# Kernel tuning notes

Hardware: AMD Instinct MI355X
Metric: run time of the kernel (lower is better)

## Reference

```python
import jax, jax.numpy as jnp
import numpy as np

B, S, D = 64, 512, 768
NEG = -1e30


def setup_inputs() -> dict:
    key = jax.random.key(0)
    ks = jax.random.split(key, 20)
    def rn(k, shape, scale=0.02):
        return jax.random.normal(k, shape, dtype=jnp.float32) * scale
    ep = jax.random.randint(ks[1], (B, 3, 2), 0, S, dtype=jnp.int32)
    return {
        "encoding": jax.random.normal(ks[0], (B, S, D), dtype=jnp.float32),
        "ent_pos": jnp.sort(ep, axis=-1),
        "Ar_W": rn(ks[2], (5, D)), "Ar_b": rn(ks[3], (D,)),
        "Vr_W1": rn(ks[4], (2 * D, 512)), "Vr_b1": rn(ks[5], (512,)),
        "Vr_W2": rn(ks[6], (512, 5)), "Vr_b2": rn(ks[7], (5,)),
        "gate_W": rn(ks[8], (2 * D, D)), "gate_b": rn(ks[9], (D,)),
        "pred_W1": rn(ks[10], (3 * D, 512)), "pred_b1": rn(ks[11], (512,)),
        "pred_W2": rn(ks[12], (512, 5)), "pred_b2": rn(ks[13], (5,)),
        "proj_W": rn(ks[14], (D, 1)), "proj_b": rn(ks[15], (1,)),
    }


def reference(encoding, ent_pos, Ar_W, Ar_b, Vr_W1, Vr_b1, Vr_W2, Vr_b2,
              gate_W, gate_b, pred_W1, pred_b1, pred_W2, pred_b2, proj_W, proj_b):
    # --- entity span max-pooling (vectorized over batch & 3 entities) ---
    pos = jnp.arange(S)                                   # [S]
    start = ent_pos[..., 0:1]                             # [B,3,1]
    end = ent_pos[..., 1:2]                               # [B,3,1]
    mask = (pos >= start) & (pos <= end)                  # [B,3,S]
    ent = jnp.max(jnp.where(mask[..., None], encoding[:, None, :, :], NEG), axis=2)  # [B,3,D]
    # dropout layers are identity at inference

    def vr(a, b):  # V_r_layer: Linear(1536,512)+ReLU+Linear(512,5)+Sigmoid
        h = jax.nn.relu(jnp.concatenate([a, b], axis=-1) @ Vr_W1 + Vr_b1)
        return jax.nn.sigmoid(h @ Vr_W2 + Vr_b2)          # [B,5]

    def gate(u, e):  # gated residual update
        g = jax.nn.sigmoid(jnp.concatenate([u, e], axis=-1) @ gate_W + gate_b)
        return g * e + (1.0 - g) * u

    e1, e2, e3 = ent[:, 0], ent[:, 1], ent[:, 2]          # [B,D] each
    for _ in range(5):
        u1 = (vr(e2, e3) @ Ar_W + Ar_b) * e1
        u2 = (vr(e1, e3) @ Ar_W + Ar_b) * e2
        u3 = (vr(e1, e2) @ Ar_W + Ar_b) * e3
        e1, e2, e3 = gate(u1, e1), gate(u2, e2), gate(u3, e3)
    final_ent = jnp.stack([e1, e2, e3], axis=1)           # [B,3,D]

    # predict_layer on the ORIGINAL pooled entity embeddings (per source code)
    flat = ent.reshape(B, 3 * D)
    rel = jax.nn.relu(flat @ pred_W1 + pred_b1) @ pred_W2 + pred_b2  # [B,5]
    ent_score = jax.nn.sigmoid(ent @ proj_W + proj_b)[..., 0]       # [B,3]
    return rel, ent_score, final_ent
```

## Files before the change

kernel.cpp:

```cpp
#include <hip/hip_runtime.h>
#include <hip/hip_bf16.h>
#include <math.h>

#define NEGF (-1e30f)

#define ENT_OFF  1179648u
#define EA_OFF   1327104u
#define EB_OFF   1474560u
#define SP_OFF   1622016u
#define PP_OFF   1637376u

__device__ __forceinline__ float sigmoidf_(float x){ return 1.0f/(1.0f+expf(-x)); }

__global__ __launch_bounds__(192) void k_span(
    const float* __restrict__ enc, const int* __restrict__ ent_pos,
    const float* __restrict__ projW, const float* __restrict__ projb,
    float* __restrict__ ws, float* __restrict__ out)
{
    __shared__ float red[4];
    int bi = blockIdx.x; int t = threadIdx.x;
    int b = bi/3;
    int st = ent_pos[bi*2+0], en = ent_pos[bi*2+1];
    float4 m = make_float4(NEGF,NEGF,NEGF,NEGF);
    const float4* e4 = (const float4*)enc + (size_t)b*512*192 + t;
    int r = st;
    for (; r+3<=en; r+=4){
        float4 v0 = e4[(size_t)(r  )*192];
        float4 v1 = e4[(size_t)(r+1)*192];
        float4 v2 = e4[(size_t)(r+2)*192];
        float4 v3 = e4[(size_t)(r+3)*192];
        m.x=fmaxf(m.x,fmaxf(fmaxf(v0.x,v1.x),fmaxf(v2.x,v3.x)));
        m.y=fmaxf(m.y,fmaxf(fmaxf(v0.y,v1.y),fmaxf(v2.y,v3.y)));
        m.z=fmaxf(m.z,fmaxf(fmaxf(v0.z,v1.z),fmaxf(v2.z,v3.z)));
        m.w=fmaxf(m.w,fmaxf(fmaxf(v0.w,v1.w),fmaxf(v2.w,v3.w)));
    }
    for (; r<=en; ++r){
        float4 v = e4[(size_t)r*192];
        m.x=fmaxf(m.x,v.x); m.y=fmaxf(m.y,v.y); m.z=fmaxf(m.z,v.z); m.w=fmaxf(m.w,v.w);
    }
    ((float4*)(ws+ENT_OFF))[bi*192+t] = m;
    ((float4*)(ws+EA_OFF))[bi*192+t] = m;
    float4 w = ((const float4*)projW)[t];
    float v = m.x*w.x + m.y*w.y + m.z*w.z + m.w*w.w;
    v += __shfl_down(v, 32);
    v += __shfl_down(v, 16);
    v += __shfl_down(v, 8);
    v += __shfl_down(v, 4);
    v += __shfl_down(v, 2);
    v += __shfl_down(v, 1);
    if ((t & 63) == 0) red[t>>6] = v;
    __syncthreads();
    if (t==0) out[320 + bi] = sigmoidf_(red[0]+red[1]+red[2] + projb[0]);
}

__global__ __launch_bounds__(256) void k_pred_part(
    const float* __restrict__ predW1, float* __restrict__ ws)
{
    int ct = blockIdx.x, rb = blockIdx.y, ks = blockIdx.z;
    int tx = threadIdx.x & 31, ty = threadIdx.x >> 5;
    int row = rb*8+ty, col = ct*32+tx;
    const float* A = ws + ENT_OFF + (size_t)row*2304 + ks*288;
    const float* W = predW1 + (size_t)(ks*288)*512 + col;
    float acc = 0.f;
    #pragma unroll 4
    for (int k=0;k<288;++k){ acc = fmaf(A[k], W[(size_t)k*512], acc); }
    ws[PP_OFF + ((size_t)(ks*64+row))*512 + col] = acc;
}

__global__ __launch_bounds__(256) void k_vr_fused(
    const float* __restrict__ W1, const float* __restrict__ b1,
    const float* __restrict__ W2, const float* __restrict__ eSrc,
    const float* __restrict__ pb1, const float* __restrict__ pW2,
    const float* __restrict__ pb2,
    float* __restrict__ ws, float* __restrict__ out)
{
    __shared__ float eL[4608];
    __shared__ float red[16*16*17];
    int g = blockIdx.x;
    int t = threadIdx.x;
    if (g >= 256){
        int bx = g - 256;
        int gid = t >> 5, l = t & 31;
        int b = bx*8 + gid;
        float acc0=0,acc1=0,acc2=0,acc3=0,acc4=0;
        for (int c = l; c < 512; c += 32){
            float h = 0.f;
            #pragma unroll
            for (int ks=0;ks<8;++ks) h += ws[PP_OFF + ((size_t)(ks*64+b))*512 + c];
            h = fmaxf(h + pb1[c], 0.f);
            acc0 = fmaf(h, pW2[c*5+0], acc0);
            acc1 = fmaf(h, pW2[c*5+1], acc1);
            acc2 = fmaf(h, pW2[c*5+2], acc2);
            acc3 = fmaf(h, pW2[c*5+3], acc3);
            acc4 = fmaf(h, pW2[c*5+4], acc4);
        }
        #pragma unroll
        for (int s=16; s>0; s>>=1){
            acc0 += __shfl_down(acc0, s, 32);
            acc1 += __shfl_down(acc1, s, 32);
            acc2 += __shfl_down(acc2, s, 32);
            acc3 += __shfl_down(acc3, s, 32);
            acc4 += __shfl_down(acc4, s, 32);
        }
        if (l == 0){
            out[b*5+0] = acc0 + pb2[0];
            out[b*5+1] = acc1 + pb2[1];
            out[b*5+2] = acc2 + pb2[2];
            out[b*5+3] = acc3 + pb2[3];
            out[b*5+4] = acc4 + pb2[4];
        }
        return;
    }
    int ct = g & 7, bg = g >> 3;
    int b0 = bg*2;
    const float* eBase = eSrc + (size_t)b0*2304;
    for (int idx=t; idx<4608; idx+=256) eL[idx] = eBase[idx];
    __syncthreads();

    int tp = t & 15;
    int kq = t >> 4;
    int c0 = ct*64;
    int col = c0 + 4*tp;
    const float* Wp = W1 + (size_t)(kq*96)*512 + col;
    int off1 = (kq<8) ? (768 + kq*96) : (1536 + (kq-8)*96);
    int off2 = (kq<8) ? (      kq*96) : (768  + (kq-8)*96);
    const float* pP0 = eL + off1;
    const float* pQ0 = eL + off2;
    const float* pP1 = eL + 2304 + off1;
    const float* pQ1 = eL + 2304 + off2;
    float aP0[4]={0,0,0,0}, aQ0[4]={0,0,0,0}, aP1[4]={0,0,0,0}, aQ1[4]={0,0,0,0};
    #pragma unroll 8
    for (int i=0;i<96;++i){
        float4 w = *(const float4*)(Wp + (size_t)i*512);
        float p0 = pP0[i], q0 = pQ0[i], p1 = pP1[i], q1 = pQ1[i];
        aP0[0]=fmaf(p0,w.x,aP0[0]); aP0[1]=fmaf(p0,w.y,aP0[1]); aP0[2]=fmaf(p0,w.z,aP0[2]); aP0[3]=fmaf(p0,w.w,aP0[3]);
        aQ0[0]=fmaf(q0,w.x,aQ0[0]); aQ0[1]=fmaf(q0,w.y,aQ0[1]); aQ0[2]=fmaf(q0,w.z,aQ0[2]); aQ0[3]=fmaf(q0,w.w,aQ0[3]);
        aP1[0]=fmaf(p1,w.x,aP1[0]); aP1[1]=fmaf(p1,w.y,aP1[1]); aP1[2]=fmaf(p1,w.z,aP1[2]); aP1[3]=fmaf(p1,w.w,aP1[3]);
        aQ1[0]=fmaf(q1,w.x,aQ1[0]); aQ1[1]=fmaf(q1,w.y,aQ1[1]); aQ1[2]=fmaf(q1,w.z,aQ1[2]); aQ1[3]=fmaf(q1,w.w,aQ1[3]);
    }
    float* rp = red + (kq*16 + tp)*17;
    #pragma unroll
    for (int c=0;c<4;++c){ rp[c]=aP0[c]; rp[4+c]=aQ0[c]; rp[8+c]=aP1[c]; rp[12+c]=aQ1[c]; }
    __syncthreads();

    if (t < 128){
        int bb = t >> 6;
        int tc = t & 63;
        int tp2 = tc >> 2, c = tc & 3;
        int base = bb*8;
        float SP1=0,SP2=0,SQ1=0,SQ2=0;
        #pragma unroll
        for (int k=0;k<8;++k){
            SP1 += red[(k*16+tp2)*17 + base + c];
            SQ1 += red[(k*16+tp2)*17 + base + 4 + c];
            SP2 += red[((k+8)*16+tp2)*17 + base + c];
            SQ2 += red[((k+8)*16+tp2)*17 + base + 4 + c];
        }
        int cc = c0 + tc;
        float bv = b1[cc];
        float h0 = fmaxf(SP1+SP2+bv, 0.f);
        float h1 = fmaxf(SQ1+SP2+bv, 0.f);
        float h2 = fmaxf(SQ1+SQ2+bv, 0.f);
        float w20 = W2[cc*5+0], w21 = W2[cc*5+1], w22 = W2[cc*5+2], w23 = W2[cc*5+3], w24 = W2[cc*5+4];
        float pr[15] = { h0*w20,h0*w21,h0*w22,h0*w23,h0*w24,
                         h1*w20,h1*w21,h1*w22,h1*w23,h1*w24,
                         h2*w20,h2*w21,h2*w22,h2*w23,h2*w24 };
        #pragma unroll
        for (int j=0;j<15;++j){
            float v = pr[j];
            v += __shfl_down(v, 32);
            v += __shfl_down(v, 16);
            v += __shfl_down(v, 8);
            v += __shfl_down(v, 4);
            v += __shfl_down(v, 2);
            v += __shfl_down(v, 1);
            pr[j] = v;
        }
        if (tc == 0){
            float* sp = ws + SP_OFF + ((size_t)ct*192 + (size_t)(b0+bb)*3)*5;
            #pragma unroll
            for (int j=0;j<15;++j) sp[j] = pr[j];
        }
    }
}

__global__ __launch_bounds__(384) void k_gate_fused(
    const float* __restrict__ gW, const float* __restrict__ gb,
    const float* __restrict__ ArW, const float* __restrict__ Arb,
    const float* __restrict__ Vb2,
    const float* __restrict__ eSrc, float* __restrict__ eDst,
    float* __restrict__ ws, float* __restrict__ finalOut)
{
    __shared__ float eL[4608];
    __shared__ float uL[4608];
    __shared__ float red[16*24*25];
    __shared__ float sL[32];
    int g = blockIdx.x;
    int t = threadIdx.x;
    int ct = g & 7, bg = g >> 3;
    int b0 = bg*2;
    const float* eBase = eSrc + (size_t)b0*2304;
    for (int idx=t; idx<4608; idx+=384) eL[idx] = eBase[idx];
    if (t < 30){
        int bb = t/15, pc = t%15, cc = pc%5;
        int row = (b0+bb)*3 + pc/5;
        float pre = Vb2[cc];
        #pragma unroll
        for (int q=0;q<8;++q) pre += ws[SP_OFF + ((size_t)q*192 + row)*5 + cc];
        sL[t] = sigmoidf_(pre);
    }
    __syncthreads();
    for (int idx=t; idx<4608; idx+=384){
        int r = idx / 768;
        int k = idx - r*768;
        int bb = r / 3;  int p = r - bb*3;
        const float* s = sL + bb*15 + p*5;
        float a = Arb[k] + s[0]*ArW[k] + s[1]*ArW[768+k] + s[2]*ArW[1536+k]
                         + s[3]*ArW[2304+k] + s[4]*ArW[3072+k];
        uL[idx] = a * eL[idx];
    }
    __syncthreads();

    int kq = t / 24, tp = t - kq*24;
    int c0 = ct*96;
    int col = c0 + 4*tp;
    const float* Wp = gW + (size_t)(kq*96)*768 + col;
    const float* A = (kq<8) ? uL : eL;
    int kb = (kq & 7)*96;
    float acc[6][4];
    #pragma unroll
    for (int r=0;r<6;++r){ acc[r][0]=0.f; acc[r][1]=0.f; acc[r][2]=0.f; acc[r][3]=0.f; }
    #pragma unroll 4
    for (int i=0;i<96;++i){
        float4 w = *(const float4*)(Wp + (size_t)i*768);
        #pragma unroll
        for (int r=0;r<6;++r){
            float a = A[r*768 + kb + i];
            acc[r][0] = fmaf(a, w.x, acc[r][0]);
            acc[r][1] = fmaf(a, w.y, acc[r][1]);
            acc[r][2] = fmaf(a, w.z, acc[r][2]);
            acc[r][3] = fmaf(a, w.w, acc[r][3]);
        }
    }
    float* rp = red + (kq*24+tp)*25;
    #pragma unroll
    for (int r=0;r<6;++r){
        rp[r*4+0]=acc[r][0]; rp[r*4+1]=acc[r][1]; rp[r*4+2]=acc[r][2]; rp[r*4+3]=acc[r][3];
    }
    __syncthreads();

    for (int o=t; o<576; o+=384){
        int rr = o / 96, tc = o - rr*96;
        int tp2 = tc >> 2, c = tc & 3;
        int bb = rr/3, p = rr - bb*3;
        float gp = 0.f;
        #pragma unroll
        for (int k=0;k<16;++k) gp += red[(k*24+tp2)*25 + rr*4 + c];
        int jc = c0 + tc;
        float gv = sigmoidf_(gp + gb[jc]);
        float e = eL[bb*2304 + p*768 + jc];
        float u = uL[bb*2304 + p*768 + jc];
        float val = gv*e + (1.f-gv)*u;
        size_t oi = ((size_t)(b0+bb)*3 + p)*768 + jc;
        eDst[oi] = val;
        if (finalOut) finalOut[oi] = val;
    }
}

extern "C" void kernel_launch(void* const* d_in, const int* in_sizes, int n_in,
                              void* d_out, int out_size, void* d_ws, size_t ws_size,
                              hipStream_t stream)
{
    const float* enc     = (const float*)d_in[0];
    const int*   ent_pos = (const int*)d_in[1];
    const float* ArW     = (const float*)d_in[2];
    const float* Arb     = (const float*)d_in[3];
    const float* VrW1    = (const float*)d_in[4];
    const float* Vrb1    = (const float*)d_in[5];
    const float* VrW2    = (const float*)d_in[6];
    const float* Vrb2    = (const float*)d_in[7];
    const float* gateW   = (const float*)d_in[8];
    const float* gateb   = (const float*)d_in[9];
    const float* predW1  = (const float*)d_in[10];
    const float* predb1  = (const float*)d_in[11];
    const float* predW2  = (const float*)d_in[12];
    const float* predb2  = (const float*)d_in[13];
    const float* projW   = (const float*)d_in[14];
    const float* projb   = (const float*)d_in[15];
    float* out = (float*)d_out;
    float* ws  = (float*)d_ws;

    hipLaunchKernelGGL(k_span, dim3(192), dim3(192), 0, stream, enc, ent_pos, projW, projb, ws, out);
    hipLaunchKernelGGL(k_pred_part, dim3(16,8,8), dim3(256), 0, stream, predW1, ws);
    for (int it=0; it<5; ++it){
        float* eS = ws + ((it&1)==0 ? EA_OFF : EB_OFF);
        float* eD = ws + ((it&1)==0 ? EB_OFF : EA_OFF);
        hipLaunchKernelGGL(k_vr_fused, dim3(it==0 ? 264 : 256), dim3(256), 0, stream,
                           VrW1, Vrb1, VrW2, eS, predb1, predW2, predb2, ws, out);
        hipLaunchKernelGGL(k_gate_fused, dim3(256), dim3(384), 0, stream, gateW, gateb, ArW, Arb, Vrb2,
                           eS, eD, ws, (it==4) ? (out+512) : (float*)nullptr);
    }
}
```

Baseline: 183.8 us.

## Split span max-pooling into chunked partial kernel plus reduce kernel

```diff
diff --git a/kernel.cpp b/kernel.cpp
--- a/kernel.cpp
+++ b/kernel.cpp
@@ -4,27 +4,27 @@
 
 #define NEGF (-1e30f)
 
-#define ENT_OFF  1179648u
-#define EA_OFF   1327104u
-#define EB_OFF   1474560u
-#define SP_OFF   1622016u
-#define PP_OFF   1637376u
+#define P_OFF    0u
+#define PP_OFF   0u
+#define ENT_OFF  2359296u
+#define EA_OFF   2506752u
+#define EB_OFF   2654208u
+#define SP_OFF   2801664u
 
 __device__ __forceinline__ float sigmoidf_(float x){ return 1.0f/(1.0f+expf(-x)); }
 
-__global__ __launch_bounds__(192) void k_span(
-    const float* __restrict__ enc, const int* __restrict__ ent_pos,
-    const float* __restrict__ projW, const float* __restrict__ projb,
-    float* __restrict__ ws, float* __restrict__ out)
-{
-    __shared__ float red[4];
-    int bi = blockIdx.x; int t = threadIdx.x;
+__global__ __launch_bounds__(192) void k_span_partial(
+    const float* __restrict__ enc, const int* __restrict__ ent_pos, float* __restrict__ ws)
+{
+    int c = blockIdx.x, bi = blockIdx.y, t = threadIdx.x;
     int b = bi/3;
     int st = ent_pos[bi*2+0], en = ent_pos[bi*2+1];
+    int r0 = max(st, c*32), r1 = min(en, c*32+31);
+    if (r0 > r1) return;
     float4 m = make_float4(NEGF,NEGF,NEGF,NEGF);
     const float4* e4 = (const float4*)enc + (size_t)b*512*192 + t;
-    int r = st;
-    for (; r+3<=en; r+=4){
+    int r = r0;
+    for (; r+3<=r1; r+=4){
         float4 v0 = e4[(size_t)(r  )*192];
         float4 v1 = e4[(size_t)(r+1)*192];
         float4 v2 = e4[(size_t)(r+2)*192];
@@ -34,9 +34,28 @@
         m.z=fmaxf(m.z,fmaxf(fmaxf(v0.z,v1.z),fmaxf(v2.z,v3.z)));
         m.w=fmaxf(m.w,fmaxf(fmaxf(v0.w,v1.w),fmaxf(v2.w,v3.w)));
     }
-    for (; r<=en; ++r){
+    for (; r<=r1; ++r){
         float4 v = e4[(size_t)r*192];
         m.x=fmaxf(m.x,v.x); m.y=fmaxf(m.y,v.y); m.z=fmaxf(m.z,v.z); m.w=fmaxf(m.w,v.w);
+    }
+    ((float4*)(ws+P_OFF))[((size_t)bi*16 + c)*192 + t] = m;
+}
+
+__global__ __launch_bounds__(192) void k_span_reduce(
+    const int* __restrict__ ent_pos,
+    const float* __restrict__ projW, const float* __restrict__ projb,
+    float* __restrict__ ws, float* __restrict__ out)
+{
+    __shared__ float red[4];
+    int bi = blockIdx.x; int t = threadIdx.x;
+    int st = ent_pos[bi*2+0], en = ent_pos[bi*2+1];
+    float4 m = make_float4(NEGF,NEGF,NEGF,NEGF);
+    const float4* p4 = (const float4*)(ws+P_OFF);
+    for (int c=0;c<16;++c){
+        if (c*32 <= en && c*32+31 >= st){
+            float4 v = p4[((size_t)bi*16 + c)*192 + t];
+            m.x=fmaxf(m.x,v.x); m.y=fmaxf(m.y,v.y); m.z=fmaxf(m.z,v.z); m.w=fmaxf(m.w,v.w);
+        }
     }
     ((float4*)(ws+ENT_OFF))[bi*192+t] = m;
     ((float4*)(ws+EA_OFF))[bi*192+t] = m;
@@ -290,7 +309,8 @@
     float* out = (float*)d_out;
     float* ws  = (float*)d_ws;
 
-    hipLaunchKernelGGL(k_span, dim3(192), dim3(192), 0, stream, enc, ent_pos, projW, projb, ws, out);
+    hipLaunchKernelGGL(k_span_partial, dim3(16,192), dim3(192), 0, stream, enc, ent_pos, ws);
+    hipLaunchKernelGGL(k_span_reduce, dim3(192), dim3(192), 0, stream, ent_pos, projW, projb, ws, out);
     hipLaunchKernelGGL(k_pred_part, dim3(16,8,8), dim3(256), 0, stream, predW1, ws);
     for (int it=0; it<5; ++it){
         float* eS = ws + ((it&1)==0 ? EA_OFF : EB_OFF);
```

New measurement: 160.2 us (median of 2 runs). 12.8% less time.
